# Kernel optimization log

Measured on AMD Instinct MI355X. Metric: run time of the kernel, lower is better.

Reference implementation:

```python
import jax, jax.numpy as jnp
import numpy as np

D_MODEL = 256
N_LEVELS = 4
N_HEADS = 8
N_POINTS = 4
LEN_Q = 1024
LEN_X = 256
SHAPES_NP = np.array([[100, 100], [50, 50], [25, 25], [13, 13]], dtype=np.int32)
LEN_IN = int((SHAPES_NP[:, 0] * SHAPES_NP[:, 1]).sum())  # 13294


def setup_inputs() -> dict:
    key = jax.random.key(0)
    ks = jax.random.split(key, 10)
    s = 0.02
    lvl_start = np.concatenate([[0], np.cumsum(SHAPES_NP[:, 0] * SHAPES_NP[:, 1])[:-1]]).astype(np.int32)
    return {
        "query": jax.random.normal(ks[0], (1, LEN_Q, D_MODEL), jnp.float32),
        "reference_points": jax.random.uniform(ks[1], (1, LEN_Q, N_LEVELS, 2), jnp.float32),
        "input_flatten": jax.random.normal(ks[2], (1, LEN_IN, D_MODEL), jnp.float32),
        "input_spatial_shapes": jnp.asarray(SHAPES_NP, jnp.int32),
        "add_keys": jax.random.normal(ks[3], (1, LEN_X, D_MODEL), jnp.float32),
        "input_level_start_index": jnp.asarray(lvl_start, jnp.int32),
        "W_off": jax.random.normal(ks[4], (N_HEADS * N_LEVELS * N_POINTS * 2, D_MODEL), jnp.float32) * s,
        "b_off": jax.random.normal(ks[5], (N_HEADS * N_LEVELS * N_POINTS * 2,), jnp.float32),
        "W_attn": jax.random.normal(ks[6], (N_HEADS * (N_LEVELS + 1), D_MODEL, D_MODEL), jnp.float32) * s,
        "W_val": jax.random.normal(ks[7], (2 * N_HEADS, D_MODEL, D_MODEL), jnp.float32) * s,
        "b_val": jax.random.normal(ks[8], (2 * N_HEADS, D_MODEL), jnp.float32) * s,
        "W_mix": jax.random.normal(ks[9], (D_MODEL, N_HEADS + 1), jnp.float32) * s,
    }


def reference(query, reference_points, input_flatten, input_spatial_shapes, add_keys,
              input_level_start_index, W_off, b_off, W_attn, W_val, b_val, W_mix):
    N, Lq, C = query.shape
    H, L, P = N_HEADS, N_LEVELS, N_POINTS

    # sampling offsets: (N, Lq, H, L, P, 2)
    off = (query @ W_off.T + b_off).reshape(N, Lq, H, L, P, 2)
    iss_f = input_spatial_shapes.astype(jnp.float32)          # (L, 2) = (H_l, W_l)
    wh = iss_f[:, ::-1]                                        # (W_l, H_l)
    loc = reference_points[:, :, None, :, None, :] + off / wh[None, None, None, :, None, :]

    # get_keys: clamp, quantize to int index (matches torch .int() trunc, values >= 0)
    loc = jnp.clip(loc, 0.0, 0.999)
    idx = (loc * iss_f[None, None, None, :, None, :]).astype(jnp.int32)
    h_l = input_spatial_shapes[:, 0]                           # (L,)
    flat_idx = (idx[..., 0] + idx[..., 1] * h_l[None, None, None, :, None]
                + input_level_start_index[None, None, None, :, None])   # (N, Lq, H, L, P)
    keys = input_flatten[0][flat_idx[0]]                       # (Lq, H, L, P, C)
    keys = jnp.transpose(keys, (1, 2, 3, 0, 4))                # (H, L, P, Lq, C)

    q = query.reshape(Lq, C)
    head_w = jax.nn.softmax(W_mix.T, axis=0)                   # (H+1, C), softmax over heads
    result = q * head_w[-1][None]
    addk = add_keys.reshape(-1, C)                             # (Lx, C)

    for h in range(H):
        attn = []
        for lvl in range(L):
            simil = W_attn[h * L + lvl]
            # faithful to torch: (C, P*Lq) row-major reshaped to (P, Lq, C)
            ki = (simil @ keys[h, lvl].reshape(-1, C).T).reshape(P, Lq, C)
            attn.append((ki * q[None]).sum(-1))                # (P, Lq)
        simil = W_attn[h * L + L]
        ki = addk @ simil.T                                    # (Lx, C)
        attn.append(ki @ q.T)                                  # (Lx, Lq)
        attn = jax.nn.softmax(jnp.concatenate(attn, axis=0), axis=0)  # (L*P+Lx, Lq)

        vals = (keys[h].reshape(-1, C) @ W_val[2 * h].T + b_val[2 * h]).reshape(L * P, Lq, C)
        v2 = addk @ W_val[2 * h + 1].T + b_val[2 * h + 1]      # (Lx, C)
        vals = jnp.concatenate([vals, jnp.broadcast_to(v2[:, None], (v2.shape[0], Lq, C))], axis=0)
        result = result + (attn[:, :, None] * vals).sum(0) * head_w[h][None]

    return result[None]
```

## Files before the change

### kernel.cpp

```cpp
#include <hip/hip_runtime.h>

typedef unsigned short ushort_t;
typedef __attribute__((ext_vector_type(8))) short bh8;
typedef __attribute__((ext_vector_type(4))) float f4;
typedef __attribute__((ext_vector_type(4))) unsigned int u4;

__device__ __forceinline__ ushort_t f2bf(float f) {
  unsigned u = __float_as_uint(f);
  return (ushort_t)((u + 0x7FFFu + ((u >> 16) & 1u)) >> 16);
}
__device__ __forceinline__ float bf2f(ushort_t v) {
  return __uint_as_float(((unsigned)v) << 16);
}

template <typename OutT>
__device__ __forceinline__ void gemm_abt_core(
    char* smem,
    const ushort_t* __restrict__ A, const ushort_t* __restrict__ B,
    OutT* __restrict__ C, int ldA, int ldB, int ldC, int K, int m0, int n0)
{
  ushort_t* As = (ushort_t*)smem;
  ushort_t* Bs = (ushort_t*)(smem + 10240);
  int t = threadIdx.x;
  int lane = t & 63, w = t >> 6;
  int quad = lane >> 4, l15 = lane & 15;
  int wm = w >> 1, wn = w & 1;
  f4 acc[4][4];
  #pragma unroll
  for (int mi = 0; mi < 4; ++mi)
    #pragma unroll
    for (int ni = 0; ni < 4; ++ni) acc[mi][ni] = (f4)0.f;
  int row = t >> 1, kh = (t & 1) * 16;
  for (int k0 = 0; k0 < K; k0 += 32) {
    if (k0) __syncthreads();
    {
      const u4* ga = (const u4*)(A + (m0 + row) * ldA + k0 + kh);
      u4 v0 = ga[0], v1 = ga[1];
      u4* da = (u4*)(As + row * 40 + kh); da[0] = v0; da[1] = v1;
      const u4* gb = (const u4*)(B + (n0 + row) * ldB + k0 + kh);
      u4 u0 = gb[0], u1 = gb[1];
      u4* db = (u4*)(Bs + row * 40 + kh); db[0] = u0; db[1] = u1;
    }
    __syncthreads();
    bh8 af[4], bfv[4];
    #pragma unroll
    for (int mi = 0; mi < 4; ++mi)
      af[mi] = *(bh8*)(As + (wm * 64 + mi * 16 + l15) * 40 + quad * 8);
    #pragma unroll
    for (int ni = 0; ni < 4; ++ni)
      bfv[ni] = *(bh8*)(Bs + (wn * 64 + ni * 16 + l15) * 40 + quad * 8);
    #pragma unroll
    for (int mi = 0; mi < 4; ++mi)
      #pragma unroll
      for (int ni = 0; ni < 4; ++ni)
        acc[mi][ni] = __builtin_amdgcn_mfma_f32_16x16x32_bf16(af[mi], bfv[ni], acc[mi][ni], 0, 0, 0);
  }
  #pragma unroll
  for (int mi = 0; mi < 4; ++mi)
    #pragma unroll
    for (int ni = 0; ni < 4; ++ni)
      #pragma unroll
      for (int r = 0; r < 4; ++r) {
        int mg = m0 + wm * 64 + mi * 16 + quad * 4 + r;
        int ng = n0 + wn * 64 + ni * 16 + l15;
        if constexpr (sizeof(OutT) == 4) C[mg * ldC + ng] = acc[mi][ni][r];
        else C[mg * ldC + ng] = (OutT)f2bf(acc[mi][ni][r]);
      }
}

__global__ __launch_bounds__(256) void k_fused_cast_off(
    const float* __restrict__ q, const float* __restrict__ xin,
    const float* __restrict__ addk, const float* __restrict__ Wval,
    const float* __restrict__ Wattn, ushort_t* __restrict__ arena,
    const float* __restrict__ Woff, float* __restrict__ off_buf)
{
  if (blockIdx.x < 2048) {
    const int total4 = 1850240;
    for (int i = blockIdx.x * 256 + threadIdx.x; i < total4; i += 2048 * 256) {
      const float* src; ushort_t* dst; int e;
      if (i < 65536)        { src = q    + i * 4;            dst = arena + i * 4; }
      else if (i < 916352)  { e = i - 65536;  src = xin  + e * 4; dst = arena + 262144  + e * 4; }
      else if (i < 932736)  { e = i - 916352; src = addk + e * 4; dst = arena + 3665408 + e * 4; }
      else if (i < 1194880) {
        e = i - 932736; int el = e * 4;
        int h = el >> 17, r = el & 131071;
        int c = r >> 9, k = r & 511;
        src = Wval + (2 * h + (k >> 8)) * 65536 + c * 256 + (k & 255);
        dst = arena + 3730944 + el;
      }
      else if (i < 1325952) {
        e = i - 1194880; int el = e * 4;
        int h = el >> 16, off = el & 65535;
        src = Wattn + h * 262144 + 262144 + off;
        dst = arena + 5828096 + el;
      }
      else {
        e = i - 1325952;
        src = Wattn + e * 4;
        dst = arena + 6352384 + e * 4;
      }
      float4 v = *(const float4*)src;
      ushort4 o; o.x = f2bf(v.x); o.y = f2bf(v.y); o.z = f2bf(v.z); o.w = f2bf(v.w);
      *(ushort4*)dst = o;
    }
  } else {
    __shared__ float As[16][65];
    __shared__ float Bs[16][65];
    int e = blockIdx.x - 2048;
    int nx = e & 3, my = e >> 2;
    int m0 = my * 64, n0 = nx * 64;
    int t = threadIdx.x;
    int tm = t & 15, tn = t >> 4;
    int lr = t >> 4, lc = t & 15;
    float acc[4][4] = {};
    for (int k0 = 0; k0 < 256; k0 += 16) {
      #pragma unroll
      for (int i = 0; i < 4; ++i) {
        int r = lr + i * 16;
        As[lc][r] = q[(m0 + r) * 256 + k0 + lc];
        Bs[lc][r] = Woff[(n0 + r) * 256 + k0 + lc];
      }
      __syncthreads();
      #pragma unroll
      for (int k = 0; k < 16; ++k) {
        float a[4], b[4];
        #pragma unroll
        for (int i = 0; i < 4; ++i) a[i] = As[k][tm * 4 + i];
        #pragma unroll
        for (int j = 0; j < 4; ++j) b[j] = Bs[k][tn * 4 + j];
        #pragma unroll
        for (int i = 0; i < 4; ++i)
          #pragma unroll
          for (int j = 0; j < 4; ++j) acc[i][j] += a[i] * b[j];
      }
      __syncthreads();
    }
    #pragma unroll
    for (int i = 0; i < 4; ++i)
      #pragma unroll
      for (int j = 0; j < 4; ++j)
        off_buf[(m0 + tm * 4 + i) * 256 + n0 + tn * 4 + j] = acc[i][j];
  }
}

__global__ __launch_bounds__(256) void k_fused_idx_g4(
    const float* __restrict__ off_buf, const float* __restrict__ boff,
    const float* __restrict__ refpts, const int* __restrict__ shapes,
    const int* __restrict__ lvlst, int* __restrict__ fidx,
    const ushort_t* __restrict__ addk, const ushort_t* __restrict__ Wattn4,
    ushort_t* __restrict__ tmp)
{
  __shared__ __align__(16) char smem[20480];
  if (blockIdx.x < 512) {
    int t = threadIdx.x;
    int b = blockIdx.x * 2 + (t >> 7), tt = t & 127;
    int l = (tt >> 2) & 3;
    float off0 = off_buf[b * 256 + 2 * tt]     + boff[2 * tt];
    float off1 = off_buf[b * 256 + 2 * tt + 1] + boff[2 * tt + 1];
    int Hi = shapes[2 * l], Wi = shapes[2 * l + 1];
    float Hf = (float)Hi, Wf = (float)Wi;
    float r0 = refpts[b * 8 + 2 * l], r1 = refpts[b * 8 + 2 * l + 1];
    float l0 = fminf(fmaxf(r0 + off0 / Wf, 0.f), 0.999f);
    float l1 = fminf(fmaxf(r1 + off1 / Hf, 0.f), 0.999f);
    int i0 = (int)(l0 * Hf);
    int i1 = (int)(l1 * Wf);
    fidx[b * 128 + tt] = i0 + i1 * Hi + lvlst[l];
  } else {
    int e = blockIdx.x - 512;
    int h = e >> 2, rem = e & 3, my = rem >> 1, nx = rem & 1;
    gemm_abt_core<ushort_t>(smem, addk, Wattn4 + h * 65536, tmp + h * 65536,
                            256, 256, 256, 256, my * 128, nx * 128);
  }
}

__device__ __forceinline__ void attn_mfma_body(
    char* smemc,
    const ushort_t* __restrict__ qbf, const ushort_t* __restrict__ xbf,
    const ushort_t* __restrict__ Wlvl, const int* __restrict__ fidx,
    float* __restrict__ attnP, int bx)
{
  unsigned* Bs = (unsigned*)smemc;
  ushort_t* As = (ushort_t*)(smemc + 8704);
  int* fis = (int*)(smemc + 17920);
  float* Nlds = (float*)smemc;

  int h = bx >> 8, l = (bx >> 6) & 3, g = bx & 63;
  int ch = g & 3, g2 = g >> 2;
  int p = g2 >> 2, tg = g2 & 3;
  int c0 = ch * 64;
  int t = threadIdx.x;
  int lane = t & 63, w = t >> 6;
  int quad = lane >> 4, l15 = lane & 15;
  int qcol = p * 4 + tg;
  fis[t] = fidx[(tg * 256 + t) * 128 + h * 16 + l * 4 + p];
  __syncthreads();
  f4 acc[4];
  #pragma unroll
  for (int mi = 0; mi < 4; ++mi) acc[mi] = (f4)0.f;

  int cl = t & 63, sg = t >> 6;
  for (int jt = 0; jt < 4; ++jt) {
    if (jt) __syncthreads();
    unsigned vv[16];
    #pragma unroll
    for (int rr = 0; rr < 16; ++rr)
      vv[rr] = xbf[fis[jt * 64 + sg * 16 + rr] * 256 + c0 + cl];
    #pragma unroll
    for (int i = 0; i < 4; ++i) {
      uint2 w2; w2.x = vv[i * 4] | (vv[i * 4 + 1] << 16);
      w2.y = vv[i * 4 + 2] | (vv[i * 4 + 3] << 16);
      *(uint2*)&Bs[cl * 34 + sg * 8 + i * 2] = w2;
    }
    {
      int u = t >> 2, jj0 = (t & 3) * 16;
      const u4* src = (const u4*)(qbf + (u * 16 + qcol) * 256 + jt * 64 + jj0);
      u4 s0 = src[0], s1 = src[1];
      u4* dst = (u4*)(As + u * 72 + jj0);
      dst[0] = s0; dst[1] = s1;
    }
    __syncthreads();
    #pragma unroll
    for (int ks = 0; ks < 2; ++ks) {
      bh8 af[4], bfv;
      #pragma unroll
      for (int mi = 0; mi < 4; ++mi)
        af[mi] = *(bh8*)(As + (mi * 16 + l15) * 72 + ks * 32 + quad * 8);
      {
        const unsigned* bp = &Bs[(w * 16 + l15) * 34 + ks * 16 + quad * 4];
        uint2 b0 = *(const uint2*)bp;
        uint2 b1 = *(const uint2*)(bp + 2);
        u4 bb; bb.x = b0.x; bb.y = b0.y; bb.z = b1.x; bb.w = b1.y;
        bfv = __builtin_bit_cast(bh8, bb);
      }
      #pragma unroll
      for (int mi = 0; mi < 4; ++mi)
        acc[mi] = __builtin_amdgcn_mfma_f32_16x16x32_bf16(af[mi], bfv, acc[mi], 0, 0, 0);
    }
  }
  __syncthreads();
  #pragma unroll
  for (int mi = 0; mi < 4; ++mi)
    *(f4*)&Nlds[(w * 16 + l15) * 68 + mi * 16 + quad * 4] = acc[mi];
  __syncthreads();
  {
    int a = t >> 6, u = t & 63;
    const ushort_t* Wr = Wlvl + (h * 4 + l) * 65536 + (a * 64 + u) * 256 + c0;
    float s = 0.f;
    #pragma unroll
    for (int cc = 0; cc < 8; ++cc) {
      u4 wv = *(const u4*)(Wr + cc * 8);
      int cb = cc * 8;
      s += __uint_as_float(wv.x << 16)         * Nlds[(cb + 0) * 68 + u];
      s += __uint_as_float(wv.x & 0xffff0000u) * Nlds[(cb + 1) * 68 + u];
      s += __uint_as_float(wv.y << 16)         * Nlds[(cb + 2) * 68 + u];
      s += __uint_as_float(wv.y & 0xffff0000u) * Nlds[(cb + 3) * 68 + u];
      s += __uint_as_float(wv.z << 16)         * Nlds[(cb + 4) * 68 + u];
      s += __uint_as_float(wv.z & 0xffff0000u) * Nlds[(cb + 5) * 68 + u];
      s += __uint_as_float(wv.w << 16)         * Nlds[(cb + 6) * 68 + u];
      s += __uint_as_float(wv.w & 0xffff0000u) * Nlds[(cb + 7) * 68 + u];
    }
    attnP[ch * 131072 + (h * 16 + l * 4 + a) * 1024 + u * 16 + qcol] = s;
  }
}

__global__ __launch_bounds__(256) void k_fused_attn(
    const ushort_t* __restrict__ qbf, const ushort_t* __restrict__ xbf,
    const ushort_t* __restrict__ Wlvl, const int* __restrict__ fidx,
    float* __restrict__ attnP,
    const ushort_t* __restrict__ tmp, float* __restrict__ attn)
{
  __shared__ __align__(16) char smem[20480];
  int bx = blockIdx.x;
  if (bx < 2048) {
    attn_mfma_body(smem, qbf, xbf, Wlvl, fidx, attnP, bx);
  } else {
    int e = bx - 2048;
    int h = e >> 4, rem = e & 15, my = rem >> 3, nx = rem & 7;
    gemm_abt_core<float>(smem, tmp + h * 65536, qbf, attn + h * 278528 + 16384,
                         256, 256, 1024, 256, my * 128, nx * 128);
  }
}

__global__ __launch_bounds__(256) void k_softmax(
    float* __restrict__ attn, const float* __restrict__ attnP,
    ushort_t* __restrict__ attn2bf, float* __restrict__ s1, float* __restrict__ s2)
{
  __shared__ float red[8][32];
  int h = blockIdx.y;
  int b = blockIdx.x * 32 + (threadIdx.x & 31);
  int rg = threadIdx.x >> 5;
  const int R0 = rg * 34;
  float* col = attn + h * 278528 + b;
  float v[34];
  float m = -1e30f;
  #pragma unroll
  for (int i = 0; i < 34; ++i) {
    int r = R0 + i;
    float x;
    if (r < 16) {
      int idx = (h * 16 + r) * 1024 + b;
      x = attnP[idx] + attnP[131072 + idx] + attnP[262144 + idx] + attnP[393216 + idx];
    } else {
      x = col[r * 1024];
    }
    v[i] = x;
    m = fmaxf(m, x);
  }
  red[rg][threadIdx.x & 31] = m;
  __syncthreads();
  #pragma unroll
  for (int j = 0; j < 8; ++j) m = fmaxf(m, red[j][threadIdx.x & 31]);
  float sum = 0.f;
  #pragma unroll
  for (int i = 0; i < 34; ++i) { v[i] = expf(v[i] - m); sum += v[i]; }
  __syncthreads();
  red[rg][threadIdx.x & 31] = sum;
  __syncthreads();
  float tot = 0.f;
  #pragma unroll
  for (int j = 0; j < 8; ++j) tot += red[j][threadIdx.x & 31];
  float inv = 1.f / tot;
  #pragma unroll
  for (int i = 0; i < 34; ++i) {
    int r = R0 + i;
    float x = v[i] * inv;
    if (r < 16) col[r * 1024] = x;
    else attn2bf[h * 262144 + (r - 16) * 1024 + b] = f2bf(x);
  }
  if (rg == 0) {
    float sa = 0.f;
    #pragma unroll
    for (int i = 0; i < 16; ++i) sa += v[i];
    float sn = sa * inv;
    s1[h * 1024 + b] = sn;
    s2[h * 1024 + b] = 1.f - sn;
  }
}

__global__ __launch_bounds__(256) void k_fused_kbar_tn(
    const ushort_t* __restrict__ xbf, const float* __restrict__ attn,
    const int* __restrict__ fidx, const ushort_t* __restrict__ attn2,
    const ushort_t* __restrict__ addk, ushort_t* __restrict__ kabar)
{
  __shared__ __align__(16) unsigned Asu[128 * 20];
  __shared__ __align__(16) unsigned Bsu[128 * 20];
  if (blockIdx.x < 1024) {
    int h = blockIdx.x >> 7, b0 = (blockIdx.x & 127) * 8;
    int t = threadIdx.x;
    int qi = t >> 5, oct = t & 31;
    int b = b0 + qi;
    float sacc[8] = {};
    #pragma unroll
    for (int r = 0; r < 16; ++r) {
      float aw = attn[(h * 272 + r) * 1024 + b];
      int row = fidx[b * 128 + h * 16 + r];
      u4 v = *(const u4*)(xbf + row * 256 + oct * 8);
      sacc[0] += aw * __uint_as_float(v.x << 16);
      sacc[1] += aw * __uint_as_float(v.x & 0xffff0000u);
      sacc[2] += aw * __uint_as_float(v.y << 16);
      sacc[3] += aw * __uint_as_float(v.y & 0xffff0000u);
      sacc[4] += aw * __uint_as_float(v.z << 16);
      sacc[5] += aw * __uint_as_float(v.z & 0xffff0000u);
      sacc[6] += aw * __uint_as_float(v.w << 16);
      sacc[7] += aw * __uint_as_float(v.w & 0xffff0000u);
    }
    u4 o;
    o.x = (unsigned)f2bf(sacc[0]) | ((unsigned)f2bf(sacc[1]) << 16);
    o.y = (unsigned)f2bf(sacc[2]) | ((unsigned)f2bf(sacc[3]) << 16);
    o.z = (unsigned)f2bf(sacc[4]) | ((unsigned)f2bf(sacc[5]) << 16);
    o.w = (unsigned)f2bf(sacc[6]) | ((unsigned)f2bf(sacc[7]) << 16);
    *(u4*)(kabar + (h * 1024 + b) * 512 + oct * 8) = o;
  } else {
    int e = blockIdx.x - 1024;
    int h = e >> 4, rem = e & 15, my = rem >> 1, nx = rem & 1;
    const ushort_t* A = attn2 + h * 262144;
    const ushort_t* B = addk;
    ushort_t* C = kabar + h * 524288;
    int m0 = my * 128, n0 = nx * 128;
    int t = threadIdx.x;
    int lane = t & 63, w = t >> 6;
    int quad = lane >> 4, l15 = lane & 15;
    int wm = w >> 1, wn = w & 1;
    f4 acc[4][4];
    #pragma unroll
    for (int mi = 0; mi < 4; ++mi)
      #pragma unroll
      for (int ni = 0; ni < 4; ++ni) acc[mi][ni] = (f4)0.f;
    int col = t & 127, half = t >> 7;
    for (int k0 = 0; k0 < 256; k0 += 32) {
      if (k0) __syncthreads();
      #pragma unroll
      for (int i = 0; i < 4; ++i) {
        int kpp = half * 4 + i;
        int kk = k0 + kpp * 4;
        unsigned x0 = A[(kk + 0) * 1024 + m0 + col];
        unsigned x1 = A[(kk + 1) * 1024 + m0 + col];
        unsigned x2 = A[(kk + 2) * 1024 + m0 + col];
        unsigned x3 = A[(kk + 3) * 1024 + m0 + col];
        uint2 va; va.x = x0 | (x1 << 16); va.y = x2 | (x3 << 16);
        *(uint2*)&Asu[col * 20 + kpp * 2] = va;
        unsigned y0 = B[(kk + 0) * 256 + n0 + col];
        unsigned y1 = B[(kk + 1) * 256 + n0 + col];
        unsigned y2 = B[(kk + 2) * 256 + n0 + col];
        unsigned y3 = B[(kk + 3) * 256 + n0 + col];
        uint2 vb; vb.x = y0 | (y1 << 16); vb.y = y2 | (y3 << 16);
        *(uint2*)&Bsu[col * 20 + kpp * 2] = vb;
      }
      __syncthreads();
      bh8 af[4], bfv[4];
      #pragma unroll
      for (int mi = 0; mi < 4; ++mi)
        af[mi] = *(bh8*)((const ushort_t*)Asu + (wm * 64 + mi * 16 + l15) * 40 + quad * 8);
      #pragma unroll
      for (int ni = 0; ni < 4; ++ni)
        bfv[ni] = *(bh8*)((const ushort_t*)Bsu + (wn * 64 + ni * 16 + l15) * 40 + quad * 8);
      #pragma unroll
      for (int mi = 0; mi < 4; ++mi)
        #pragma unroll
        for (int ni = 0; ni < 4; ++ni)
          acc[mi][ni] = __builtin_amdgcn_mfma_f32_16x16x32_bf16(af[mi], bfv[ni], acc[mi][ni], 0, 0, 0);
    }
    #pragma unroll
    for (int mi = 0; mi < 4; ++mi)
      #pragma unroll
      for (int ni = 0; ni < 4; ++ni)
        #pragma unroll
        for (int r = 0; r < 4; ++r) {
          int mg = m0 + wm * 64 + mi * 16 + quad * 4 + r;
          int ng = n0 + wn * 64 + ni * 16 + l15;
          C[mg * 512 + 256 + ng] = f2bf(acc[mi][ni][r]);
        }
  }
}

__global__ __launch_bounds__(256) void gemm_val_k(
    const ushort_t* __restrict__ kabar, const ushort_t* __restrict__ Wcat,
    float* __restrict__ Y)
{
  __shared__ __align__(16) char smem[20480];
  int h = blockIdx.z;
  gemm_abt_core<float>(smem, kabar + h * 524288, Wcat + h * 131072, Y + h * 262144,
                       512, 512, 256, 512, blockIdx.y * 128, blockIdx.x * 128);
}

__global__ __launch_bounds__(256) void k_combine(
    const float* __restrict__ q, const float* __restrict__ Wmix,
    const float* __restrict__ Y,
    const float* __restrict__ s1, const float* __restrict__ s2,
    const float* __restrict__ bval, float* __restrict__ out)
{
  int b = blockIdx.x, c = threadIdx.x;
  float w[9];
  float m = -1e30f;
  #pragma unroll
  for (int j = 0; j < 9; ++j) { w[j] = Wmix[c * 9 + j]; m = fmaxf(m, w[j]); }
  float tot = 0.f;
  #pragma unroll
  for (int j = 0; j < 9; ++j) { w[j] = expf(w[j] - m); tot += w[j]; }
  float inv = 1.f / tot;
  float res = q[b * 256 + c] * w[8] * inv;
  #pragma unroll
  for (int hh = 0; hh < 8; ++hh) {
    float y = Y[(hh * 1024 + b) * 256 + c]
            + s1[hh * 1024 + b] * bval[(2 * hh) * 256 + c]
            + s2[hh * 1024 + b] * bval[(2 * hh + 1) * 256 + c];
    res += w[hh] * inv * y;
  }
  out[b * 256 + c] = res;
}

extern "C" void kernel_launch(void* const* d_in, const int* in_sizes, int n_in,
                              void* d_out, int out_size, void* d_ws, size_t ws_size,
                              hipStream_t stream) {
  (void)in_sizes; (void)n_in; (void)out_size; (void)ws_size;
  const float* q      = (const float*)d_in[0];
  const float* refpts = (const float*)d_in[1];
  const float* xin    = (const float*)d_in[2];
  const int*   shapes = (const int*)d_in[3];
  const float* addk   = (const float*)d_in[4];
  const int*   lvlst  = (const int*)d_in[5];
  const float* Woff   = (const float*)d_in[6];
  const float* boff   = (const float*)d_in[7];
  const float* Wattn  = (const float*)d_in[8];
  const float* Wval   = (const float*)d_in[9];
  const float* bval   = (const float*)d_in[10];
  const float* Wmix   = (const float*)d_in[11];
  float* out = (float*)d_out;
  float* ws  = (float*)d_ws;

  int*   fidx    = (int*)ws;
  float* off_buf = ws + 131072;
  float* s1      = ws + 393216;
  float* s2      = ws + 401408;
  float* attn    = ws + 409600;
  float* Y       = ws + 409600;
  ushort_t* arena = (ushort_t*)(ws + 2637824);
  ushort_t* q_bf     = arena;
  ushort_t* xin_bf   = arena + 262144;
  ushort_t* addk_bf  = arena + 3665408;
  ushort_t* Wcat_bf  = arena + 3730944;
  ushort_t* Wattn4_bf= arena + 5828096;
  ushort_t* Wlvl_bf  = arena + 6352384;
  ushort_t* tmp_bf   = arena + 8449536;
  ushort_t* attn2_bf = arena + 8973824;
  ushort_t* kabar_bf = arena + 11070976;
  float* attnP = (float*)(arena + 15265280);

  k_fused_cast_off<<<2112, 256, 0, stream>>>(q, xin, addk, Wval, Wattn, arena,
                                             Woff, off_buf);
  k_fused_idx_g4<<<544, 256, 0, stream>>>(off_buf, boff, refpts, shapes, lvlst,
                                          fidx, addk_bf, Wattn4_bf, tmp_bf);
  k_fused_attn<<<2176, 256, 0, stream>>>(q_bf, xin_bf, Wlvl_bf, fidx, attnP,
                                         tmp_bf, attn);
  k_softmax<<<dim3(32, 8), 256, 0, stream>>>(attn, attnP, attn2_bf, s1, s2);
  k_fused_kbar_tn<<<1152, 256, 0, stream>>>(xin_bf, attn, fidx, attn2_bf,
                                            addk_bf, kabar_bf);
  gemm_val_k<<<dim3(2, 8, 8), 256, 0, stream>>>(kabar_bf, Wcat_bf, Y);
  k_combine<<<1024, 256, 0, stream>>>(q, Wmix, Y, s1, s2, bval, out);
}
```

Baseline: 206.8 us.

## Merge offset/index and addk-Wattn GEMM stages into one launch

Folds the second kernel into the first: the sampling-offset projection and the index computation now run together in one per-query block path, and the addk×Wattn (extra level) product is computed directly from fp32 inputs with an FP32 tiled GEMM instead of first casting Wattn to bf16 and running an MFMA GEMM. This drops one kernel launch, the off_buf round-trip and the Wattn4 cast traffic. In exchange the small GEMM runs on scalar FP32 ALUs rather than matrix cores, and the per-query offset dot products read Woff from global memory without tiling.

```diff
diff --git a/kernel.cpp b/kernel.cpp
--- a/kernel.cpp
+++ b/kernel.cpp
@@ -68,15 +68,20 @@
       }
 }
 
-__global__ __launch_bounds__(256) void k_fused_cast_off(
+__global__ __launch_bounds__(256) void k_stage1(
     const float* __restrict__ q, const float* __restrict__ xin,
     const float* __restrict__ addk, const float* __restrict__ Wval,
     const float* __restrict__ Wattn, ushort_t* __restrict__ arena,
-    const float* __restrict__ Woff, float* __restrict__ off_buf)
-{
-  if (blockIdx.x < 2048) {
-    const int total4 = 1850240;
-    for (int i = blockIdx.x * 256 + threadIdx.x; i < total4; i += 2048 * 256) {
+    const float* __restrict__ Woff, const float* __restrict__ boff,
+    const float* __restrict__ refpts, const int* __restrict__ shapes,
+    const int* __restrict__ lvlst, int* __restrict__ fidx,
+    ushort_t* __restrict__ tmp)
+{
+  __shared__ __align__(16) float smem[2 * 16 * 65];
+  int bx = blockIdx.x;
+  if (bx < 2048) {
+    const int total4 = 1719168;
+    for (int i = bx * 256 + threadIdx.x; i < total4; i += 2048 * 256) {
       const float* src; ushort_t* dst; int e;
       if (i < 65536)        { src = q    + i * 4;            dst = arena + i * 4; }
       else if (i < 916352)  { e = i - 65536;  src = xin  + e * 4; dst = arena + 262144  + e * 4; }
@@ -88,14 +93,8 @@
         src = Wval + (2 * h + (k >> 8)) * 65536 + c * 256 + (k & 255);
         dst = arena + 3730944 + el;
       }
-      else if (i < 1325952) {
-        e = i - 1194880; int el = e * 4;
-        int h = el >> 16, off = el & 65535;
-        src = Wattn + h * 262144 + 262144 + off;
-        dst = arena + 5828096 + el;
-      }
       else {
-        e = i - 1325952;
+        e = i - 1194880;
         src = Wattn + e * 4;
         dst = arena + 6352384 + e * 4;
       }
@@ -103,22 +102,56 @@
       ushort4 o; o.x = f2bf(v.x); o.y = f2bf(v.y); o.z = f2bf(v.z); o.w = f2bf(v.w);
       *(ushort4*)dst = o;
     }
+  } else if (bx < 2560) {
+    int b2 = bx - 2048;
+    int t = threadIdx.x;
+    smem[t]       = q[b2 * 512 + t];
+    smem[t + 256] = q[b2 * 512 + 256 + t];
+    __syncthreads();
+    int qh = t >> 7, tt = t & 127;
+    const float* qs = smem + qh * 256;
+    const float* w0 = Woff + (2 * tt) * 256;
+    const float* w1 = w0 + 256;
+    float o0 = 0.f, o1 = 0.f;
+    #pragma unroll 4
+    for (int d = 0; d < 256; d += 4) {
+      float4 a = *(const float4*)(qs + d);
+      float4 x = *(const float4*)(w0 + d);
+      float4 y = *(const float4*)(w1 + d);
+      o0 += a.x * x.x + a.y * x.y + a.z * x.z + a.w * x.w;
+      o1 += a.x * y.x + a.y * y.y + a.z * y.z + a.w * y.w;
+    }
+    int b = b2 * 2 + qh;
+    int l = (tt >> 2) & 3;
+    float off0 = o0 + boff[2 * tt];
+    float off1 = o1 + boff[2 * tt + 1];
+    int Hi = shapes[2 * l], Wi = shapes[2 * l + 1];
+    float Hf = (float)Hi, Wf = (float)Wi;
+    float r0 = refpts[b * 8 + 2 * l], r1 = refpts[b * 8 + 2 * l + 1];
+    float l0 = fminf(fmaxf(r0 + off0 / Wf, 0.f), 0.999f);
+    float l1 = fminf(fmaxf(r1 + off1 / Hf, 0.f), 0.999f);
+    int i0 = (int)(l0 * Hf);
+    int i1 = (int)(l1 * Wf);
+    fidx[b * 128 + tt] = i0 + i1 * Hi + lvlst[l];
   } else {
-    __shared__ float As[16][65];
-    __shared__ float Bs[16][65];
-    int e = blockIdx.x - 2048;
-    int nx = e & 3, my = e >> 2;
-    int m0 = my * 64, n0 = nx * 64;
+    int e = bx - 2560;
+    int h = e >> 4, tile = e & 15;
+    int m0 = (tile >> 2) * 64, n0 = (tile & 3) * 64;
+    const float* A = addk;
+    const float* B = Wattn + h * 262144 + 262144;
+    float (*As)[65] = (float(*)[65])smem;
+    float (*Bs)[65] = (float(*)[65])(smem + 16 * 65);
     int t = threadIdx.x;
     int tm = t & 15, tn = t >> 4;
     int lr = t >> 4, lc = t & 15;
     float acc[4][4] = {};
     for (int k0 = 0; k0 < 256; k0 += 16) {
+      if (k0) __syncthreads();
       #pragma unroll
       for (int i = 0; i < 4; ++i) {
         int r = lr + i * 16;
-        As[lc][r] = q[(m0 + r) * 256 + k0 + lc];
-        Bs[lc][r] = Woff[(n0 + r) * 256 + k0 + lc];
+        As[lc][r] = A[(m0 + r) * 256 + k0 + lc];
+        Bs[lc][r] = B[(n0 + r) * 256 + k0 + lc];
       }
       __syncthreads();
       #pragma unroll
@@ -133,43 +166,13 @@
           #pragma unroll
           for (int j = 0; j < 4; ++j) acc[i][j] += a[i] * b[j];
       }
-      __syncthreads();
-    }
+    }
+    ushort_t* Cb = tmp + h * 65536;
     #pragma unroll
     for (int i = 0; i < 4; ++i)
       #pragma unroll
       for (int j = 0; j < 4; ++j)
-        off_buf[(m0 + tm * 4 + i) * 256 + n0 + tn * 4 + j] = acc[i][j];
-  }
-}
-
-__global__ __launch_bounds__(256) void k_fused_idx_g4(
-    const float* __restrict__ off_buf, const float* __restrict__ boff,
-    const float* __restrict__ refpts, const int* __restrict__ shapes,
-    const int* __restrict__ lvlst, int* __restrict__ fidx,
-    const ushort_t* __restrict__ addk, const ushort_t* __restrict__ Wattn4,
-    ushort_t* __restrict__ tmp)
-{
-  __shared__ __align__(16) char smem[20480];
-  if (blockIdx.x < 512) {
-    int t = threadIdx.x;
-    int b = blockIdx.x * 2 + (t >> 7), tt = t & 127;
-    int l = (tt >> 2) & 3;
-    float off0 = off_buf[b * 256 + 2 * tt]     + boff[2 * tt];
-    float off1 = off_buf[b * 256 + 2 * tt + 1] + boff[2 * tt + 1];
-    int Hi = shapes[2 * l], Wi = shapes[2 * l + 1];
-    float Hf = (float)Hi, Wf = (float)Wi;
-    float r0 = refpts[b * 8 + 2 * l], r1 = refpts[b * 8 + 2 * l + 1];
-    float l0 = fminf(fmaxf(r0 + off0 / Wf, 0.f), 0.999f);
-    float l1 = fminf(fmaxf(r1 + off1 / Hf, 0.f), 0.999f);
-    int i0 = (int)(l0 * Hf);
-    int i1 = (int)(l1 * Wf);
-    fidx[b * 128 + tt] = i0 + i1 * Hi + lvlst[l];
-  } else {
-    int e = blockIdx.x - 512;
-    int h = e >> 2, rem = e & 3, my = rem >> 1, nx = rem & 1;
-    gemm_abt_core<ushort_t>(smem, addk, Wattn4 + h * 65536, tmp + h * 65536,
-                            256, 256, 256, 256, my * 128, nx * 128);
+        Cb[(m0 + tm * 4 + i) * 256 + n0 + tn * 4 + j] = f2bf(acc[i][j]);
   }
 }
 
@@ -489,7 +492,6 @@
   float* ws  = (float*)d_ws;
 
   int*   fidx    = (int*)ws;
-  float* off_buf = ws + 131072;
   float* s1      = ws + 393216;
   float* s2      = ws + 401408;
   float* attn    = ws + 409600;
@@ -499,17 +501,15 @@
   ushort_t* xin_bf   = arena + 262144;
   ushort_t* addk_bf  = arena + 3665408;
   ushort_t* Wcat_bf  = arena + 3730944;
-  ushort_t* Wattn4_bf= arena + 5828096;
   ushort_t* Wlvl_bf  = arena + 6352384;
   ushort_t* tmp_bf   = arena + 8449536;
   ushort_t* attn2_bf = arena + 8973824;
   ushort_t* kabar_bf = arena + 11070976;
   float* attnP = (float*)(arena + 15265280);
 
-  k_fused_cast_off<<<2112, 256, 0, stream>>>(q, xin, addk, Wval, Wattn, arena,
-                                             Woff, off_buf);
-  k_fused_idx_g4<<<544, 256, 0, stream>>>(off_buf, boff, refpts, shapes, lvlst,
-                                          fidx, addk_bf, Wattn4_bf, tmp_bf);
+  k_stage1<<<2688, 256, 0, stream>>>(q, xin, addk, Wval, Wattn, arena,
+                                     Woff, boff, refpts, shapes, lvlst,
+                                     fidx, tmp_bf);
   k_fused_attn<<<2176, 256, 0, stream>>>(q_bf, xin_bf, Wlvl_bf, fidx, attnP,
                                          tmp_bf, attn);
   k_softmax<<<dim3(32, 8), 256, 0, stream>>>(attn, attnP, attn2_bf, s1, s2);
```

Measured after the change: 231.3 us. 11.8% more time.
